# Kernel optimization log

Hardware: AMD Instinct MI355X
Metric: run time of the kernel (lower is better)

The kernel has to match this reference:

```python
import jax, jax.numpy as jnp
import numpy as np
jax.config.update("jax_enable_x64", True)

HASH_PRIMES = [2654435761, 2246822519, 3266489917, 2028178513, 1220703125, 1610612741,
               805306457, 402653189, 3674653429, 2860486313, 1073676287, 2971215073,
               1500450271, 3267000013, 2654435789, 4049292737]
SCALE_WINDOWS = [1, 2, 4, 8]

VOCAB = 1024
BUCKETS = 4_000_000
NUM_SCALES = 4
E = 4                 # embed_per_scale
BOUNDARY = 2          # condition_boundary (min(2, num_scales))
SIGN_BITS = 8
BATCH, T = 32, 2048


def _hash_scale(tokens, scale_idx):
    # rolling shift-xor-mul hash over a small fixed window (<=8)
    window = SCALE_WINDOWS[scale_idx]
    primes = HASH_PRIMES[:window]
    h = jnp.zeros_like(tokens)
    Tlen = tokens.shape[1]
    for i in range(window):
        off = i + 1
        if off >= Tlen:
            continue
        shifted = jnp.pad(tokens[:, :-off], ((0, 0), (off, 0)))  # zeros at front
        h = h ^ (shifted * primes[i])
    return h % BUCKETS


def setup_inputs() -> dict:
    key = jax.random.key(0)
    ks = jax.random.split(key, 6)
    tokens = jax.random.randint(ks[0], (BATCH, T), 0, VOCAB, dtype=jnp.int64)
    tables = [0.02 * jax.random.normal(ks[1 + s], (BUCKETS, E), dtype=jnp.float32)
              for s in range(NUM_SCALES)]
    # nn.Linear(short_dim=BOUNDARY*E, SIGN_BITS, bias=False): weight [out, in]
    short_dim = BOUNDARY * E
    bound = 1.0 / np.sqrt(short_dim)
    cond_w = jax.random.uniform(ks[5], (SIGN_BITS, short_dim),
                                minval=-bound, maxval=bound, dtype=jnp.float32)
    return {"tokens": tokens, "table0": tables[0], "table1": tables[1],
            "table2": tables[2], "table3": tables[3], "cond_w": cond_w}


def reference(tokens, table0, table1, table2, table3, cond_w):
    tables = [table0, table1, table2, table3]
    keys = [_hash_scale(tokens, s) for s in range(NUM_SCALES)]
    # short scales: plain hashed gather
    short_embeds = [tables[s][keys[s]] for s in range(BOUNDARY)]  # [B,T,E] each
    # condition long scales on short-scale sign bits
    short_cat = jnp.concatenate(short_embeds, axis=-1)            # [B,T,BOUNDARY*E]
    cond_logits = jnp.einsum('btd,od->bto', short_cat, cond_w)    # [B,T,SIGN_BITS]
    sign_bits = (cond_logits > 0).astype(jnp.int64)
    cond_key = jnp.zeros(tokens.shape, dtype=jnp.int64)
    for i in range(SIGN_BITS):
        cond_key = cond_key ^ (sign_bits[:, :, i] * HASH_PRIMES[i])
    long_embeds = []
    for s in range(BOUNDARY, NUM_SCALES):
        k = (keys[s] ^ cond_key) % BUCKETS
        long_embeds.append(tables[s][k])
    return jnp.concatenate(short_embeds + long_embeds, axis=-1)   # [B,T,NUM_SCALES*E]
```

## Files before the change

kernel.cpp:

```cpp
#include <hip/hip_runtime.h>
#include <cstdint>


constexpr int TT = 2048;
constexpr int BB = 32;
constexpr uint32_t BUCKETS = 4000000u;

__device__ constexpr uint64_t PRIMES64[8] = {
    2654435761ull, 2246822519ull, 3266489917ull, 2028178513ull,
    1220703125ull, 1610612741ull,  805306457ull,  402653189ull};

extern "C" __global__ void __launch_bounds__(256)
pyramid_kernel(const int* __restrict__ tokens,
               const float* __restrict__ t0,
               const float* __restrict__ t1,
               const float* __restrict__ t2,
               const float* __restrict__ t3,
               const float* __restrict__ cw,
               float* __restrict__ out)
{
    __shared__ int   stok[264];
    __shared__ float scw[64];

    const int tid          = threadIdx.x;
    const int blocksPerRow = TT / 256;
    const int b            = blockIdx.x / blocksPerRow;
    const int tBase        = (blockIdx.x % blocksPerRow) * 256;
    const int* row         = tokens + (size_t)b * TT;

    for (int i = tid; i < 264; i += 256) {
        const int t = tBase - 8 + i;
        stok[i] = (t >= 0) ? row[t] : 0;
    }
    if (tid < 64) scw[tid] = cw[tid];
    __syncthreads();

    const int t = tBase + tid;

    uint64_t x = 0;
    x ^= (uint64_t)(uint32_t)stok[tid + 7] * PRIMES64[0];
    const uint32_t k0 = (uint32_t)(x % BUCKETS);
    x ^= (uint64_t)(uint32_t)stok[tid + 6] * PRIMES64[1];
    const uint32_t k1 = (uint32_t)(x % BUCKETS);
    x ^= (uint64_t)(uint32_t)stok[tid + 5] * PRIMES64[2];
    x ^= (uint64_t)(uint32_t)stok[tid + 4] * PRIMES64[3];
    const uint32_t k2h = (uint32_t)(x % BUCKETS);
    x ^= (uint64_t)(uint32_t)stok[tid + 3] * PRIMES64[4];
    x ^= (uint64_t)(uint32_t)stok[tid + 2] * PRIMES64[5];
    x ^= (uint64_t)(uint32_t)stok[tid + 1] * PRIMES64[6];
    x ^= (uint64_t)(uint32_t)stok[tid + 0] * PRIMES64[7];
    const uint32_t k3h = (uint32_t)(x % BUCKETS);

    const float4 e0 = *(const float4*)(t0 + (size_t)k0 * 4);
    const float4 e1 = *(const float4*)(t1 + (size_t)k1 * 4);

    const float cat[8] = {e0.x, e0.y, e0.z, e0.w, e1.x, e1.y, e1.z, e1.w};
    uint32_t ck = 0;
#pragma unroll
    for (int o = 0; o < 8; ++o) {
        float acc = 0.f;
#pragma unroll
        for (int d = 0; d < 8; ++d) acc = fmaf(cat[d], scw[o * 8 + d], acc);
        if (acc > 0.f) ck ^= (uint32_t)PRIMES64[o];
    }

    const uint32_t kk2 = (k2h ^ ck) % BUCKETS;
    const uint32_t kk3 = (k3h ^ ck) % BUCKETS;
    const float4 e2 = *(const float4*)(t2 + (size_t)kk2 * 4);
    const float4 e3 = *(const float4*)(t3 + (size_t)kk3 * 4);

    float4* o4 = (float4*)(out + (size_t)(b * TT + t) * 16);
    o4[0] = e0; o4[1] = e1; o4[2] = e2; o4[3] = e3;
}

extern "C" void kernel_launch(void* const* d_in, const int* in_sizes, int n_in,
                              void* d_out, int out_size, void* d_ws, size_t ws_size,
                              hipStream_t stream)
{
    const int*   tokens = (const int*)d_in[0];
    const float* t0     = (const float*)d_in[1];
    const float* t1     = (const float*)d_in[2];
    const float* t2     = (const float*)d_in[3];
    const float* t3     = (const float*)d_in[4];
    const float* cw     = (const float*)d_in[5];
    float*       out    = (float*)d_out;

    const dim3 grid(BB * (TT / 256));
    pyramid_kernel<<<grid, 256, 0, stream>>>(tokens, t0, t1, t2, t3, cw, out);
}
```

Baseline: 186.9 us.

## Split each token across four lanes for gathers and coalesced output stores

Each token is now handled by four lanes instead of one. Two lanes gather the short-scale embeddings, the sign bits are rebuilt from them through wavefront shuffles, and each lane writes one float4 so the output stores become contiguous and coalesced. The intent is more memory-level parallelism and better store coalescing. The cost is that every lane recomputes the full 64-bit hash chain and modulo, and some lanes issue redundant gathers: lanes 2/3 repeat the short gathers and lanes 0/1 repeat the long ones.

```diff
diff --git a/kernel.cpp b/kernel.cpp
--- a/kernel.cpp
+++ b/kernel.cpp
@@ -5,6 +5,7 @@
 constexpr int TT = 2048;
 constexpr int BB = 32;
 constexpr uint32_t BUCKETS = 4000000u;
+constexpr int ELEMS_PER_BLOCK = 64;
 
 __device__ constexpr uint64_t PRIMES64[8] = {
     2654435761ull, 2246822519ull, 3266489917ull, 2028178513ull,
@@ -19,42 +20,55 @@
                const float* __restrict__ cw,
                float* __restrict__ out)
 {
-    __shared__ int   stok[264];
+    __shared__ int   stok[ELEMS_PER_BLOCK + 8];
     __shared__ float scw[64];
 
-    const int tid          = threadIdx.x;
-    const int blocksPerRow = TT / 256;
-    const int b            = blockIdx.x / blocksPerRow;
-    const int tBase        = (blockIdx.x % blocksPerRow) * 256;
-    const int* row         = tokens + (size_t)b * TT;
+    const int tid = threadIdx.x;
+    const int el  = tid >> 2;
+    const int r   = tid & 3;
 
-    for (int i = tid; i < 264; i += 256) {
-        const int t = tBase - 8 + i;
-        stok[i] = (t >= 0) ? row[t] : 0;
+    const int blocksPerRow = TT / ELEMS_PER_BLOCK;
+    const int b     = blockIdx.x / blocksPerRow;
+    const int tBase = (blockIdx.x % blocksPerRow) * ELEMS_PER_BLOCK;
+    const int* row  = tokens + (size_t)b * TT;
+
+    if (tid < ELEMS_PER_BLOCK + 8) {
+        const int t = tBase - 8 + tid;
+        stok[tid] = (t >= 0) ? row[t] : 0;
     }
     if (tid < 64) scw[tid] = cw[tid];
     __syncthreads();
 
-    const int t = tBase + tid;
-
     uint64_t x = 0;
-    x ^= (uint64_t)(uint32_t)stok[tid + 7] * PRIMES64[0];
+    x ^= (uint64_t)(uint32_t)stok[el + 7] * PRIMES64[0];
     const uint32_t k0 = (uint32_t)(x % BUCKETS);
-    x ^= (uint64_t)(uint32_t)stok[tid + 6] * PRIMES64[1];
+    x ^= (uint64_t)(uint32_t)stok[el + 6] * PRIMES64[1];
     const uint32_t k1 = (uint32_t)(x % BUCKETS);
-    x ^= (uint64_t)(uint32_t)stok[tid + 5] * PRIMES64[2];
-    x ^= (uint64_t)(uint32_t)stok[tid + 4] * PRIMES64[3];
+    x ^= (uint64_t)(uint32_t)stok[el + 5] * PRIMES64[2];
+    x ^= (uint64_t)(uint32_t)stok[el + 4] * PRIMES64[3];
     const uint32_t k2h = (uint32_t)(x % BUCKETS);
-    x ^= (uint64_t)(uint32_t)stok[tid + 3] * PRIMES64[4];
-    x ^= (uint64_t)(uint32_t)stok[tid + 2] * PRIMES64[5];
-    x ^= (uint64_t)(uint32_t)stok[tid + 1] * PRIMES64[6];
-    x ^= (uint64_t)(uint32_t)stok[tid + 0] * PRIMES64[7];
+    x ^= (uint64_t)(uint32_t)stok[el + 3] * PRIMES64[4];
+    x ^= (uint64_t)(uint32_t)stok[el + 2] * PRIMES64[5];
+    x ^= (uint64_t)(uint32_t)stok[el + 1] * PRIMES64[6];
+    x ^= (uint64_t)(uint32_t)stok[el + 0] * PRIMES64[7];
     const uint32_t k3h = (uint32_t)(x % BUCKETS);
 
-    const float4 e0 = *(const float4*)(t0 + (size_t)k0 * 4);
-    const float4 e1 = *(const float4*)(t1 + (size_t)k1 * 4);
+    const float*  sp = (r & 1) ? t1 : t0;
+    const uint32_t sk = (r & 1) ? k1 : k0;
+    const float4 v1 = *(const float4*)(sp + (size_t)sk * 4);
 
-    const float cat[8] = {e0.x, e0.y, e0.z, e0.w, e1.x, e1.y, e1.z, e1.w};
+    const int wl   = threadIdx.x & 63;
+    const int base = wl & ~3;
+    float cat[8];
+    cat[0] = __shfl(v1.x, base + 0, 64);
+    cat[1] = __shfl(v1.y, base + 0, 64);
+    cat[2] = __shfl(v1.z, base + 0, 64);
+    cat[3] = __shfl(v1.w, base + 0, 64);
+    cat[4] = __shfl(v1.x, base + 1, 64);
+    cat[5] = __shfl(v1.y, base + 1, 64);
+    cat[6] = __shfl(v1.z, base + 1, 64);
+    cat[7] = __shfl(v1.w, base + 1, 64);
+
     uint32_t ck = 0;
 #pragma unroll
     for (int o = 0; o < 8; ++o) {
@@ -66,11 +80,13 @@
 
     const uint32_t kk2 = (k2h ^ ck) % BUCKETS;
     const uint32_t kk3 = (k3h ^ ck) % BUCKETS;
-    const float4 e2 = *(const float4*)(t2 + (size_t)kk2 * 4);
-    const float4 e3 = *(const float4*)(t3 + (size_t)kk3 * 4);
+    const float*   lp  = (r & 1) ? t3 : t2;
+    const uint32_t lk  = (r & 1) ? kk3 : kk2;
+    const float4 v2 = *(const float4*)(lp + (size_t)lk * 4);
 
-    float4* o4 = (float4*)(out + (size_t)(b * TT + t) * 16);
-    o4[0] = e0; o4[1] = e1; o4[2] = e2; o4[3] = e3;
+    const float4 vo = (r < 2) ? v1 : v2;
+    const int elemG = b * TT + tBase + el;
+    *(float4*)(out + (size_t)elemG * 16 + r * 4) = vo;
 }
 
 extern "C" void kernel_launch(void* const* d_in, const int* in_sizes, int n_in,
@@ -85,6 +101,6 @@
     const float* cw     = (const float*)d_in[5];
     float*       out    = (float*)d_out;
 
-    const dim3 grid(BB * (TT / 256));
+    const dim3 grid(BB * (TT / ELEMS_PER_BLOCK));
     pyramid_kernel<<<grid, 256, 0, stream>>>(tokens, t0, t1, t2, t3, cw, out);
 }
```

Measured after the change: 186.2 us. About the same (-0.4%).
